# Kernel optimization log

Measured on AMD Instinct MI355X. Metric: run time of the kernel, lower is better.

Reference implementation:

```python
import jax, jax.numpy as jnp
import numpy as np


def setup_inputs() -> dict:
    key = jax.random.key(0)
    B, C, H, W = 16, 512, 56, 56
    heads, agent, win = 8, 49, 56
    ks = jax.random.split(key, 16)
    std = 0.02
    tn = lambda k, s: jax.random.truncated_normal(k, -2.0, 2.0, s, jnp.float32) * std
    return {
        "x": jax.random.normal(ks[0], (B, C, H, W), jnp.float32),
        "H": H,
        "W": W,
        "q_w": jax.random.normal(ks[1], (C, C), jnp.float32) * (C ** -0.5),
        "kv_w": jax.random.normal(ks[2], (2 * C, C), jnp.float32) * (C ** -0.5),
        "proj_w": jax.random.normal(ks[3], (C, C), jnp.float32) * (C ** -0.5),
        "proj_b": jnp.zeros((C,), jnp.float32),
        "dwc_w": jax.random.normal(ks[4], (C, 1, 3, 3), jnp.float32) * (1.0 / 3.0),
        "dwc_b": jnp.zeros((C,), jnp.float32),
        "an_bias": tn(ks[5], (heads, agent, 7, 7)),
        "na_bias": tn(ks[6], (heads, agent, 7, 7)),
        "ah_bias": tn(ks[7], (1, heads, agent, win, 1)),
        "aw_bias": tn(ks[8], (1, heads, agent, 1, win)),
        "ha_bias": tn(ks[9], (1, heads, win, 1, agent)),
        "wa_bias": tn(ks[10], (1, heads, 1, win, agent)),
    }


def reference(x, H, W, q_w, kv_w, proj_w, proj_b, dwc_w, dwc_b,
              an_bias, na_bias, ah_bias, aw_bias, ha_bias, wa_bias):
    B, C, H1, W1 = x.shape
    heads, agent = an_bias.shape[0], an_bias.shape[1]
    hd = C // heads
    scale = hd ** -0.5
    n = H1 * W1
    pool = int(agent ** 0.5)  # 7

    # NOTE: original torch code does x.view(B, H1*W1, C) on an NCHW tensor:
    # a raw row-major reshape, reproduced faithfully here.
    xf = x.reshape(B, n, C)

    q = xf @ q_w.T                       # [B, n, C]
    kv = xf @ kv_w.T                     # [B, n, 2C]
    k, v = kv[..., :C], kv[..., C:]

    # agent tokens: adaptive avg pool of q (as HxW image) to pool x pool (exact blocks)
    q_img = q.reshape(B, H, W, C)
    agent_tokens = q_img.reshape(B, pool, H // pool, pool, W // pool, C).mean(axis=(2, 4))
    agent_tokens = agent_tokens.reshape(B, agent, C)

    qh = q.reshape(B, n, heads, hd).transpose(0, 2, 1, 3)            # [B,h,n,d]
    kh = k.reshape(B, n, heads, hd).transpose(0, 2, 1, 3)            # [B,h,n,d]
    vh = v.reshape(B, n, heads, hd).transpose(0, 2, 1, 3)            # [B,h,n,d]
    ah = agent_tokens.reshape(B, agent, heads, hd).transpose(0, 2, 1, 3)  # [B,h,a,d]

    # stage 1: agent -> kv attention, with interpolated + separable position bias
    pb1 = jax.image.resize(an_bias, (heads, agent, H, W), 'bilinear').reshape(1, heads, agent, n)
    pb2 = (ah_bias + aw_bias).reshape(1, heads, agent, n)
    agent_logits = jnp.einsum('bhad,bhnd->bhan', ah * scale, kh) + pb1 + pb2
    agent_attn = jax.nn.softmax(agent_logits, axis=-1)
    agent_v = jnp.einsum('bhan,bhnd->bhad', agent_attn, vh)          # [B,h,a,d]

    # stage 2: query -> agent attention
    ab1 = jax.image.resize(na_bias, (heads, agent, H, W), 'bilinear').reshape(1, heads, agent, n)
    ab1 = ab1.transpose(0, 1, 3, 2)                                  # [1,h,n,a]
    ab2 = (ha_bias + wa_bias).reshape(1, heads, n, agent)
    q_logits = jnp.einsum('bhnd,bhad->bhna', qh * scale, ah) + ab1 + ab2
    q_attn = jax.nn.softmax(q_logits, axis=-1)
    out = jnp.einsum('bhna,bhad->bhnd', q_attn, agent_v)
    out = out.transpose(0, 2, 1, 3).reshape(B, n, C)

    # depthwise-conv residual on v (sr_ratio == 1: no interpolate)
    v_img = v.reshape(B, H, W, C).transpose(0, 3, 1, 2)              # [B,C,H,W]
    dwc = jax.lax.conv_general_dilated(
        v_img, dwc_w, window_strides=(1, 1), padding='SAME',
        feature_group_count=C, dimension_numbers=('NCHW', 'OIHW', 'NCHW'))
    dwc = dwc + dwc_b[None, :, None, None]
    out = out + dwc.transpose(0, 2, 3, 1).reshape(B, n, C)

    out = out @ proj_w.T + proj_b
    return out.reshape(B, C, H1, W1)
```

## Files before the change

### kernel.cpp

```cpp
#include <hip/hip_runtime.h>
#include <math.h>

#define B_ 16
#define C_ 512
#define Nn 3136
#define HEADS 8
#define HD 64
#define AG 49
#define Mrows (B_ * Nn)

typedef unsigned short ushortT;
typedef __attribute__((ext_vector_type(8))) short bf16x8;
typedef __attribute__((ext_vector_type(4))) float f32x4;

#define MFMA16(a, b, c) __builtin_amdgcn_mfma_f32_16x16x32_bf16((a), (b), (c), 0, 0, 0)

__device__ inline float bf2f(ushortT u) { return __uint_as_float(((unsigned)u) << 16); }
__device__ inline ushortT f2bf(float f) {
    unsigned x = __float_as_uint(f);
    unsigned r = (x + 0x7fffu + ((x >> 16) & 1u)) >> 16;
    return (ushortT)r;
}
__device__ inline f32x4 fzero4() { f32x4 z = {0.f, 0.f, 0.f, 0.f}; return z; }

__device__ inline void gl_lds16(const ushortT* g, ushortT* l) {
    __builtin_amdgcn_global_load_lds(
        (const __attribute__((address_space(1))) void*)g,
        (__attribute__((address_space(3))) void*)l, 16, 0, 0);
}

#define VMCNT(n) asm volatile("s_waitcnt vmcnt(" #n ")" ::: "memory")
#define LGKM0_SB() { asm volatile("s_waitcnt lgkmcnt(0)" ::: "memory"); \
                     __builtin_amdgcn_sched_barrier(0); }
#define BAR() __builtin_amdgcn_s_barrier()

__global__ void cvt_f2b4(const float* __restrict__ src, ushortT* __restrict__ dst, int n4) {
    int g = blockIdx.x * 256 + threadIdx.x;
    if (g >= n4) return;
    float4 v = *(const float4*)&src[(size_t)g * 4];
    ushort4 o = make_ushort4(f2bf(v.x), f2bf(v.y), f2bf(v.z), f2bf(v.w));
    *(ushort4*)&dst[(size_t)g * 4] = o;
}

__global__ void cvt_weights(const float* __restrict__ qw, const float* __restrict__ kvw,
                            const float* __restrict__ pw, const float* __restrict__ dwcw,
                            ushortT* __restrict__ Wqkv, ushortT* __restrict__ Wp,
                            float* __restrict__ wT) {
    int g = blockIdx.x * 256 + threadIdx.x;
    if (g < 196608) {
        const float* src = (g < 65536) ? &qw[(size_t)g * 4] : &kvw[(size_t)(g - 65536) * 4];
        float4 v = *(const float4*)src;
        *(ushort4*)&Wqkv[(size_t)g * 4] =
            make_ushort4(f2bf(v.x), f2bf(v.y), f2bf(v.z), f2bf(v.w));
    } else if (g < 262144) {
        float4 v = *(const float4*)&pw[(size_t)(g - 196608) * 4];
        *(ushort4*)&Wp[(size_t)(g - 196608) * 4] =
            make_ushort4(f2bf(v.x), f2bf(v.y), f2bf(v.z), f2bf(v.w));
    } else {
        int gg = g - 262144;
        if (gg < 4608) { int c = gg & 511, tap = gg >> 9; wT[gg] = dwcw[c * 9 + tap]; }
    }
}

template <int MB, int NL>
__device__ __forceinline__ void quad(f32x4 (&acc)[8][4], const bf16x8 (&af)[4][2],
                                     const bf16x8 (&bf)[4][2]) {
#pragma unroll
    for (int m = 0; m < 4; ++m)
#pragma unroll
        for (int n = 0; n < 2; ++n) {
            acc[MB + m][NL + n] = MFMA16(af[m][0], bf[NL + n][0], acc[MB + m][NL + n]);
            acc[MB + m][NL + n] = MFMA16(af[m][1], bf[NL + n][1], acc[MB + m][NL + n]);
        }
}

template <typename TO>
__global__ __launch_bounds__(512, 2)
void gemm256(const ushortT* __restrict__ A, const ushortT* __restrict__ Bw,
             const float* __restrict__ bias, TO* __restrict__ out,
             int N, int nbn) {
    __shared__ __align__(16) ushortT As[2][16384];
    __shared__ __align__(16) ushortT Bs[2][16384];
    const int t = threadIdx.x, lane = t & 63, wid = t >> 6;
    const int chunk = (int)gridDim.x >> 3;
    const int id2 = ((int)blockIdx.x & 7) * chunk + ((int)blockIdx.x >> 3);
    const int by = id2 / nbn, bx = id2 - by * nbn;
    const int m0 = by * 256, n0 = bx * 256;
    const int wm = wid >> 2, wn = wid & 3;

    const int rl0 = t >> 3;
    const int skg = (t & 7) ^ (rl0 & 7);
    const int ra0 = rl0 & 63;
    const int ra1 = (rl0 & 63) + 128;
    const int rb0 = (rl0 & 31) + ((rl0 >> 5) << 6);
    const int rb1 = rb0 + 128;
    const ushortT* gA0 = A + (size_t)(m0 + ra0) * 512 + skg * 8;
    const ushortT* gA1 = A + (size_t)(m0 + ra1) * 512 + skg * 8;
    const ushortT* gB0 = Bw + (size_t)(n0 + rb0) * 512 + skg * 8;
    const ushortT* gB1 = Bw + (size_t)(n0 + rb1) * 512 + skg * 8;
    const int bA0 = wid * 512;
    const int bA1 = wid * 512 + 8192;
    const int gbu = ((wid * 8) & 31) + (((wid * 8) >> 5) << 6);
    const int bB0 = gbu * 64;
    const int bB1 = bB0 + 8192;

#define ISSA(bufi, ro, ko) { gl_lds16(gA0 + (ro) * 512 + (ko), &As[bufi][bA0 + (ro) * 64]); \
                             gl_lds16(gA1 + (ro) * 512 + (ko), &As[bufi][bA1 + (ro) * 64]); }
#define ISSB(bufi, ro, ko) { gl_lds16(gB0 + (ro) * 512 + (ko), &Bs[bufi][bB0 + (ro) * 64]); \
                             gl_lds16(gB1 + (ro) * 512 + (ko), &Bs[bufi][bB1 + (ro) * 64]); }

    f32x4 acc[8][4];
#pragma unroll
    for (int i = 0; i < 8; ++i)
#pragma unroll
        for (int j = 0; j < 4; ++j) acc[i][j] = fzero4();

    const int r15 = lane & 15, kq16 = lane >> 4;
    const int rA = wm * 128 + r15;
    const int rB = wn * 64 + r15;
    const int sw0 = ((kq16) ^ (r15 & 7)) << 3;
    const int sw1 = ((4 + kq16) ^ (r15 & 7)) << 3;

    ISSA(0, 0, 0); ISSA(0, 64, 0);
    ISSB(0, 0, 0); ISSB(0, 32, 0);
    VMCNT(0);
    BAR();

    bf16x8 af[4][2], bf[4][2];
    for (int kt = 0; kt < 8; ++kt) {
        const ushortT* Ac = As[kt & 1];
        const ushortT* Bc = Bs[kt & 1];
        const int nb = (kt + 1) & 1;
        const int ko = (kt + 1) * 64;
        const bool pre = (kt < 7);
#pragma unroll
        for (int mt = 0; mt < 4; ++mt) {
            af[mt][0] = *(const bf16x8*)&Ac[(rA + mt * 16) * 64 + sw0];
            af[mt][1] = *(const bf16x8*)&Ac[(rA + mt * 16) * 64 + sw1];
        }
#pragma unroll
        for (int nt = 0; nt < 2; ++nt) {
            bf[nt][0] = *(const bf16x8*)&Bc[(rB + nt * 16) * 64 + sw0];
            bf[nt][1] = *(const bf16x8*)&Bc[(rB + nt * 16) * 64 + sw1];
        }
        if (pre) { ISSA(nb, 0, ko); ISSA(nb, 64, ko); }
        BAR(); LGKM0_SB();
        __builtin_amdgcn_s_setprio(1);
        quad<0, 0>(acc, af, bf);
        __builtin_amdgcn_s_setprio(0);
        BAR();
#pragma unroll
        for (int nt = 2; nt < 4; ++nt) {
            bf[nt][0] = *(const bf16x8*)&Bc[(rB + nt * 16) * 64 + sw0];
            bf[nt][1] = *(const bf16x8*)&Bc[(rB + nt * 16) * 64 + sw1];
        }
        if (pre) { ISSB(nb, 0, ko); ISSB(nb, 32, ko); }
        BAR(); LGKM0_SB();
        __builtin_amdgcn_s_setprio(1);
        quad<0, 2>(acc, af, bf);
        __builtin_amdgcn_s_setprio(0);
        BAR();
#pragma unroll
        for (int mt = 0; mt < 4; ++mt) {
            af[mt][0] = *(const bf16x8*)&Ac[(rA + 64 + mt * 16) * 64 + sw0];
            af[mt][1] = *(const bf16x8*)&Ac[(rA + 64 + mt * 16) * 64 + sw1];
        }
        BAR(); LGKM0_SB();
        __builtin_amdgcn_s_setprio(1);
        quad<4, 0>(acc, af, bf);
        __builtin_amdgcn_s_setprio(0);
        BAR();
        __builtin_amdgcn_s_setprio(1);
        quad<4, 2>(acc, af, bf);
        __builtin_amdgcn_s_setprio(0);
        if (pre) { VMCNT(0); }
        BAR();
    }
#undef ISSA
#undef ISSB

    const int cn = r15, rg = kq16 << 2;
#pragma unroll
    for (int mt = 0; mt < 8; ++mt) {
        int mrow = m0 + wm * 128 + mt * 16 + rg;
#pragma unroll
        for (int nt = 0; nt < 4; ++nt) {
            int ncol = n0 + wn * 64 + nt * 16 + cn;
            float bv = bias ? bias[ncol] : 0.f;
#pragma unroll
            for (int r = 0; r < 4; ++r) {
                float v = acc[mt][nt][r] + bv;
                if (sizeof(TO) == 2) ((ushortT*)out)[(size_t)(mrow + r) * N + ncol] = f2bf(v);
                else                 ((float*)out)[(size_t)(mrow + r) * N + ncol] = v;
            }
        }
    }
}

__global__ __launch_bounds__(256)
void agent_pool(const ushortT* __restrict__ qkv, float* __restrict__ at) {
    __shared__ float red[256][9];
    int t = threadIdx.x;
    int ba = blockIdx.x;
    int b = ba / AG, a = ba % AG;
    int c8 = (t & 63) << 3, qr = t >> 6;
    int p1 = a / 7, p2 = a % 7;
    float s[8] = {};
#pragma unroll
    for (int pp = 0; pp < 16; ++pp) {
        int pos = (qr << 4) + pp;
        int i = (p1 * 8 + (pos >> 3)) * 56 + p2 * 8 + (pos & 7);
        bf16x8 u = *(const bf16x8*)&qkv[(size_t)(b * Nn + i) * 1536 + c8];
#pragma unroll
        for (int j = 0; j < 8; ++j) s[j] += bf2f((ushortT)u[j]);
    }
#pragma unroll
    for (int j = 0; j < 8; ++j) red[t][j] = s[j];
    __syncthreads();
    if (t < 64) {
        float* o = &at[((size_t)(b * AG + a) << 9) + (t << 3)];
#pragma unroll
        for (int j = 0; j < 8; ++j)
            o[j] = (red[t][j] + red[t + 64][j] + red[t + 128][j] + red[t + 192][j])
                   * (1.f / 64.f);
    }
}

__device__ inline float bilin7(const float* __restrict__ p, int y, int x) {
    float fy = fminf(fmaxf(y * 0.125f - 0.4375f, 0.f), 6.f);
    float fx = fminf(fmaxf(x * 0.125f - 0.4375f, 0.f), 6.f);
    int y0 = (int)fy; float ty = fy - y0; int y1 = min(y0 + 1, 6);
    int x0 = (int)fx; float tx = fx - x0; int x1 = min(x0 + 1, 6);
    float v00 = p[y0 * 7 + x0], v01 = p[y0 * 7 + x1];
    float v10 = p[y1 * 7 + x0], v11 = p[y1 * 7 + x1];
    return (1.f - ty) * ((1.f - tx) * v00 + tx * v01) + ty * ((1.f - tx) * v10 + tx * v11);
}

__global__ void bias_k(const float* __restrict__ an, const float* __restrict__ ahb,
                       const float* __restrict__ awb, const float* __restrict__ na,
                       const float* __restrict__ hab, const float* __restrict__ wab,
                       float* __restrict__ b1, float* __restrict__ b2) {
    int g = blockIdx.x * 256 + threadIdx.x;
    const int NT = HEADS * AG * Nn;
    if (g < NT) {
        int i = g % Nn; int a = (g / Nn) % AG; int h = g / (AG * Nn);
        int y = i / 56, x = i % 56;
        b1[g] = bilin7(an + (h * AG + a) * 49, y, x)
              + ahb[(h * AG + a) * 56 + y] + awb[(h * AG + a) * 56 + x];
    } else {
        g -= NT; if (g >= NT) return;
        int a = g % AG; int i = (g / AG) % Nn; int h = g / (AG * Nn);
        int y = i / 56, x = i % 56;
        b2[g] = bilin7(na + (h * AG + a) * 49, y, x)
              + hab[(h * 56 + y) * AG + a] + wab[(h * 56 + x) * AG + a];
    }
}

__global__ void zero2(float* __restrict__ num, int n1, float* __restrict__ den, int n2) {
    int g = blockIdx.x * 256 + threadIdx.x;
    if (g < n1) num[g] = 0.f;
    else if (g - n1 < n2) den[g - n1] = 0.f;
}

__global__ __launch_bounds__(256)
void agent_av_fused(const ushortT* __restrict__ qkv, const float* __restrict__ at,
                    const float* __restrict__ b1, float* __restrict__ num,
                    float* __restrict__ den) {
    __shared__ __align__(16) ushortT ah_s[64 * 72];
    __shared__ __align__(16) ushortT vt[64 * 72];
    __shared__ __align__(16) ushortT p_s[64 * 72];
    const int t = threadIdx.x, lane = t & 63, wid = t >> 6;
    const int bh = blockIdx.y, b = bh >> 3, h = bh & 7;
    for (int idx = t; idx < 512; idx += 256) {
        int a = idx >> 3, d8 = (idx & 7) << 3;
        bf16x8 tmp;
        if (a < AG) {
            const float* p = &at[((size_t)(b * AG + a) << 9) + (h << 6) + d8];
#pragma unroll
            for (int j = 0; j < 8; ++j) tmp[j] = (short)f2bf(p[j] * 0.125f);
        } else {
#pragma unroll
            for (int j = 0; j < 8; ++j) tmp[j] = 0;
        }
        *(bf16x8*)&ah_s[a * 72 + d8] = tmp;
    }
    __syncthreads();
    const int r15 = lane & 15, kq = (lane >> 4) << 3;
    const int rbase = (lane >> 4) << 2;
    bf16x8 af[4][2];
#pragma unroll
    for (int mt = 0; mt < 4; ++mt)
#pragma unroll
        for (int ks = 0; ks < 2; ++ks)
            af[mt][ks] = *(const bf16x8*)&ah_s[(mt * 16 + r15) * 72 + ks * 32 + kq];

    f32x4 accn[4];
#pragma unroll
    for (int nt = 0; nt < 4; ++nt) accn[nt] = fzero4();
    float denl[4][4];
#pragma unroll
    for (int mt = 0; mt < 4; ++mt)
#pragma unroll
        for (int r = 0; r < 4; ++r) denl[mt][r] = 0.f;

    const int i0b = blockIdx.x * 448;
    const int svi = t >> 2, svd = (t & 3) << 4;
    for (int cc = 0; cc < 7; ++cc) {
        const int i0 = i0b + cc * 64;
        {
            const ushortT* vp = &qkv[(size_t)(b * Nn + i0 + svi) * 1536 + 1024 + (h << 6) + svd];
            bf16x8 u0 = *(const bf16x8*)vp;
            bf16x8 u1 = *(const bf16x8*)(vp + 8);
#pragma unroll
            for (int j = 0; j < 8; ++j) {
                vt[(svd + j) * 72 + svi]     = (ushortT)u0[j];
                vt[(svd + 8 + j) * 72 + svi] = (ushortT)u1[j];
            }
        }
        {
            const int iw = i0 + wid * 16;
            const ushortT* kp = &qkv[(size_t)(b * Nn + iw + r15) * 1536 + 512 + (h << 6) + kq];
            bf16x8 bk0 = *(const bf16x8*)kp;
            bf16x8 bk1 = *(const bf16x8*)(kp + 32);
            f32x4 sacc[4];
#pragma unroll
            for (int mt = 0; mt < 4; ++mt) {
                sacc[mt] = MFMA16(af[mt][0], bk0, fzero4());
                sacc[mt] = MFMA16(af[mt][1], bk1, sacc[mt]);
            }
            const int ic = iw + r15;
#pragma unroll
            for (int mt = 0; mt < 4; ++mt)
#pragma unroll
                for (int r = 0; r < 4; ++r) {
                    int a = mt * 16 + rbase + r;
                    float e = 0.f;
                    if (a < AG)
                        e = __expf(sacc[mt][r] + b1[(size_t)(h * AG + a) * Nn + ic]);
                    denl[mt][r] += e;
                    p_s[a * 72 + wid * 16 + r15] = f2bf(e);
                }
        }
        __syncthreads();
        {
            bf16x8 ap0 = *(const bf16x8*)&p_s[(wid * 16 + r15) * 72 + kq];
            bf16x8 ap1 = *(const bf16x8*)&p_s[(wid * 16 + r15) * 72 + 32 + kq];
#pragma unroll
            for (int nt = 0; nt < 4; ++nt) {
                bf16x8 bv0 = *(const bf16x8*)&vt[(nt * 16 + r15) * 72 + kq];
                bf16x8 bv1 = *(const bf16x8*)&vt[(nt * 16 + r15) * 72 + 32 + kq];
                accn[nt] = MFMA16(ap0, bv0, accn[nt]);
                accn[nt] = MFMA16(ap1, bv1, accn[nt]);
            }
        }
        __syncthreads();
    }
#pragma unroll
    for (int r = 0; r < 4; ++r) {
        int a = wid * 16 + rbase + r;
        if (a < AG) {
#pragma unroll
            for (int nt = 0; nt < 4; ++nt)
                atomicAdd(&num[((size_t)(bh * AG + a) << 6) + nt * 16 + r15],
                          accn[nt][r]);
        }
    }
#pragma unroll
    for (int mt = 0; mt < 4; ++mt)
#pragma unroll
        for (int r = 0; r < 4; ++r) {
            float s = denl[mt][r];
#pragma unroll
            for (int off = 8; off >= 1; off >>= 1) s += __shfl_xor(s, off);
            if (r15 == 0) {
                int a = mt * 16 + rbase + r;
                if (a < AG) atomicAdd(&den[bh * AG + a], s);
            }
        }
}

__global__ __launch_bounds__(256)
void q_attn_mfma(const ushortT* __restrict__ qkv, const float* __restrict__ at,
                 const float* __restrict__ num, const float* __restrict__ den,
                 const float* __restrict__ b2, ushortT* __restrict__ attn) {
    __shared__ __align__(16) ushortT ah_s[64 * 72];
    __shared__ __align__(16) ushortT avT[64 * 72];
    __shared__ __align__(16) ushortT p_s[4][16 * 72];
    int t = threadIdx.x, lane = t & 63, wid = t >> 6;
    int bh = blockIdx.y, b = bh >> 3, h = bh & 7;
    for (int idx = t; idx < 512; idx += 256) {
        int a = idx >> 3, d8 = (idx & 7) << 3;
        bf16x8 tmp;
        if (a < AG) {
            const float* p = &at[((size_t)(b * AG + a) << 9) + (h << 6) + d8];
#pragma unroll
            for (int j = 0; j < 8; ++j) tmp[j] = (short)f2bf(p[j] * 0.125f);
        } else {
#pragma unroll
            for (int j = 0; j < 8; ++j) tmp[j] = 0;
        }
        *(bf16x8*)&ah_s[a * 72 + d8] = tmp;
    }
    for (int idx = t; idx < 4096; idx += 256) {
        int a = idx >> 6, d = idx & 63;
        float v = 0.f;
        if (a < AG)
            v = num[((size_t)(bh * AG + a) << 6) + d] / den[bh * AG + a];
        avT[d * 72 + a] = f2bf(v);
    }
    __syncthreads();
    int r15 = lane & 15, kq = (lane >> 4) << 3;
    bf16x8 bah[4][2], bav[4][2];
#pragma unroll
    for (int nt = 0; nt < 4; ++nt)
#pragma unroll
        for (int ks = 0; ks < 2; ++ks) {
            bah[nt][ks] = *(const bf16x8*)&ah_s[(nt * 16 + r15) * 72 + ks * 32 + kq];
            bav[nt][ks] = *(const bf16x8*)&avT[(nt * 16 + r15) * 72 + ks * 32 + kq];
        }
    ushortT* psw = p_s[wid];
    int i0b = blockIdx.x * 448;
    int rbase = (lane >> 4) << 2;
    for (int tt = 0; tt < 7; ++tt) {
        int i0 = i0b + (wid * 7 + tt) * 16;
        const ushortT* qp = &qkv[(size_t)(b * Nn + i0 + r15) * 1536 + (h << 6) + kq];
        bf16x8 aq0 = *(const bf16x8*)qp;
        bf16x8 aq1 = *(const bf16x8*)(qp + 32);
        f32x4 lg[4];
#pragma unroll
        for (int nt = 0; nt < 4; ++nt) {
            lg[nt] = MFMA16(aq0, bah[nt][0], fzero4());
            lg[nt] = MFMA16(aq1, bah[nt][1], lg[nt]);
        }
        float p4[4][4];
#pragma unroll
        for (int r = 0; r < 4; ++r) {
            int i = i0 + rbase + r;
            float vals[4]; float sm = 0.f;
#pragma unroll
            for (int nt = 0; nt < 4; ++nt) {
                int a = nt * 16 + r15;
                float e = 0.f;
                if (a < AG) e = __expf(lg[nt][r] + b2[(size_t)(h * Nn + i) * AG + a]);
                vals[nt] = e; sm += e;
            }
#pragma unroll
            for (int off = 8; off >= 1; off >>= 1) sm += __shfl_xor(sm, off);
            float inv = 1.f / sm;
#pragma unroll
            for (int nt = 0; nt < 4; ++nt) p4[nt][r] = vals[nt] * inv;
        }
#pragma unroll
        for (int nt = 0; nt < 4; ++nt)
#pragma unroll
            for (int r = 0; r < 4; ++r)
                psw[(rbase + r) * 72 + nt * 16 + r15] = f2bf(p4[nt][r]);
        bf16x8 ap0 = *(const bf16x8*)&psw[r15 * 72 + kq];
        bf16x8 ap1 = *(const bf16x8*)&psw[r15 * 72 + 32 + kq];
        f32x4 ov[4];
#pragma unroll
        for (int nt = 0; nt < 4; ++nt) {
            ov[nt] = MFMA16(ap0, bav[nt][0], fzero4());
            ov[nt] = MFMA16(ap1, bav[nt][1], ov[nt]);
        }
#pragma unroll
        for (int r = 0; r < 4; ++r) {
            int i = i0 + rbase + r;
            ushortT* op = &attn[(size_t)(b * Nn + i) * C_ + (h << 6)];
#pragma unroll
            for (int nt = 0; nt < 4; ++nt)
                op[nt * 16 + r15] = f2bf(ov[nt][r]);
        }
    }
}

__global__ void dwc_add_v(const ushortT* __restrict__ qkv, const float* __restrict__ wT,
                          const float* __restrict__ bb, ushortT* __restrict__ attn) {
    int g = blockIdx.x * 256 + threadIdx.x;
    int c8 = (g & 63) << 3;
    int bi = g >> 6;
    int i = bi % Nn;
    int y = i / 56, x = i % 56;
    float acc[8];
    {
        float4 b0 = *(const float4*)&bb[c8];
        float4 b1 = *(const float4*)&bb[c8 + 4];
        acc[0] = b0.x; acc[1] = b0.y; acc[2] = b0.z; acc[3] = b0.w;
        acc[4] = b1.x; acc[5] = b1.y; acc[6] = b1.z; acc[7] = b1.w;
    }
#pragma unroll
    for (int dy = -1; dy <= 1; ++dy) {
        int yy = y + dy; if (yy < 0 || yy > 55) continue;
#pragma unroll
        for (int dx = -1; dx <= 1; ++dx) {
            int xx = x + dx; if (xx < 0 || xx > 55) continue;
            const ushortT* vp = &qkv[(size_t)(bi + dy * 56 + dx) * 1536 + 1024 + c8];
            ushort4 u0 = *(const ushort4*)vp;
            ushort4 u1 = *(const ushort4*)(vp + 4);
            const float* wp = &wT[((dy + 1) * 3 + dx + 1) * 512 + c8];
            float4 w0 = *(const float4*)wp;
            float4 w1 = *(const float4*)(wp + 4);
            acc[0] += bf2f(u0.x) * w0.x; acc[1] += bf2f(u0.y) * w0.y;
            acc[2] += bf2f(u0.z) * w0.z; acc[3] += bf2f(u0.w) * w0.w;
            acc[4] += bf2f(u1.x) * w1.x; acc[5] += bf2f(u1.y) * w1.y;
            acc[6] += bf2f(u1.z) * w1.z; acc[7] += bf2f(u1.w) * w1.w;
        }
    }
    ushortT* op = &attn[(size_t)bi * C_ + c8];
    ushort4 a0 = *(const ushort4*)op;
    ushort4 a1 = *(const ushort4*)(op + 4);
    ushort4 o0 = make_ushort4(f2bf(bf2f(a0.x) + acc[0]), f2bf(bf2f(a0.y) + acc[1]),
                              f2bf(bf2f(a0.z) + acc[2]), f2bf(bf2f(a0.w) + acc[3]));
    ushort4 o1 = make_ushort4(f2bf(bf2f(a1.x) + acc[4]), f2bf(bf2f(a1.y) + acc[5]),
                              f2bf(bf2f(a1.z) + acc[6]), f2bf(bf2f(a1.w) + acc[7]));
    *(ushort4*)op = o0; *(ushort4*)(op + 4) = o1;
}

extern "C" void kernel_launch(void* const* d_in, const int* in_sizes, int n_in,
                              void* d_out, int out_size, void* d_ws, size_t ws_size,
                              hipStream_t stream) {
    const float* x      = (const float*)d_in[0];
    const float* q_w    = (const float*)d_in[3];
    const float* kv_w   = (const float*)d_in[4];
    const float* proj_w = (const float*)d_in[5];
    const float* proj_b = (const float*)d_in[6];
    const float* dwc_w  = (const float*)d_in[7];
    const float* dwc_b  = (const float*)d_in[8];
    const float* an_b   = (const float*)d_in[9];
    const float* na_b   = (const float*)d_in[10];
    const float* ah_b   = (const float*)d_in[11];
    const float* aw_b   = (const float*)d_in[12];
    const float* ha_b   = (const float*)d_in[13];
    const float* wa_b   = (const float*)d_in[14];
    float* out = (float*)d_out;

    char* ws = (char*)d_ws;
    ushortT* R    = (ushortT*)(ws);
    ushortT* qkv  = (ushortT*)(ws + 51380224);
    ushortT* Wqkv = (ushortT*)(ws + 205520896);
    ushortT* Wp   = (ushortT*)(ws + 207093760);
    float*   wT   = (float*)(ws + 207618048);
    float*   at   = (float*)(ws + 207636480);
    float*   b1   = (float*)(ws + 209242112);
    float*   b2   = (float*)(ws + 214159360);
    float*   num  = (float*)(ws + 219076608);
    float*   den  = (float*)Wqkv;
    ushortT* xb   = R;
    ushortT* attn = R;

    cvt_f2b4<<<25088, 256, 0, stream>>>(x, xb, 6422528);
    cvt_weights<<<1042, 256, 0, stream>>>(q_w, kv_w, proj_w, dwc_w, Wqkv, Wp, wT);
    gemm256<ushortT><<<1176, 512, 0, stream>>>(xb, Wqkv, nullptr, qkv, 1536, 6);
    agent_pool<<<784, 256, 0, stream>>>(qkv, at);
    bias_k<<<9604, 256, 0, stream>>>(an_b, ah_b, aw_b, na_b, ha_b, wa_b, b1, b2);
    zero2<<<1593, 256, 0, stream>>>(num, B_ * HEADS * AG * HD, den, B_ * HEADS * AG);
    agent_av_fused<<<dim3(7, 128), 256, 0, stream>>>(qkv, at, b1, num, den);
    q_attn_mfma<<<dim3(7, 128), 256, 0, stream>>>(qkv, at, num, den, b2, attn);
    dwc_add_v<<<12544, 256, 0, stream>>>(qkv, wT, dwc_b, attn);
    gemm256<float><<<392, 512, 0, stream>>>(attn, Wp, proj_b, out, 512, 2);
}
```

Measured before the change: 527.5 us.

## Use 128x128 GEMM tiles, bf16 bias/agent buffers, and atomic-free partial reductions

Replaces the 256x256 eight-wave GEMM with a simpler 128x128 four-wave GEMM that has a single barrier per k-step and more blocks. Agent tokens and the bias tables are stored as bf16 instead of fp32, with the head scale folded into the pooling, which halves their memory traffic. The agent-attention kernel now writes per-chunk partial numerators and denominators instead of using atomics, so the zeroing kernel is removed and q_attn sums the four partials. The smaller GEMM tile lowers data reuse per block, and bf16 biases reduce accuracy slightly.

```diff
diff --git a/kernel.cpp b/kernel.cpp
--- a/kernel.cpp
+++ b/kernel.cpp
@@ -30,8 +30,6 @@
 }
 
 #define VMCNT(n) asm volatile("s_waitcnt vmcnt(" #n ")" ::: "memory")
-#define LGKM0_SB() { asm volatile("s_waitcnt lgkmcnt(0)" ::: "memory"); \
-                     __builtin_amdgcn_sched_barrier(0); }
 #define BAR() __builtin_amdgcn_s_barrier()
 
 __global__ void cvt_f2b4(const float* __restrict__ src, ushortT* __restrict__ dst, int n4) {
@@ -62,67 +60,49 @@
     }
 }
 
-template <int MB, int NL>
-__device__ __forceinline__ void quad(f32x4 (&acc)[8][4], const bf16x8 (&af)[4][2],
-                                     const bf16x8 (&bf)[4][2]) {
-#pragma unroll
-    for (int m = 0; m < 4; ++m)
-#pragma unroll
-        for (int n = 0; n < 2; ++n) {
-            acc[MB + m][NL + n] = MFMA16(af[m][0], bf[NL + n][0], acc[MB + m][NL + n]);
-            acc[MB + m][NL + n] = MFMA16(af[m][1], bf[NL + n][1], acc[MB + m][NL + n]);
-        }
-}
-
 template <typename TO>
-__global__ __launch_bounds__(512, 2)
-void gemm256(const ushortT* __restrict__ A, const ushortT* __restrict__ Bw,
+__global__ __launch_bounds__(256, 2)
+void gemm128(const ushortT* __restrict__ A, const ushortT* __restrict__ Bw,
              const float* __restrict__ bias, TO* __restrict__ out,
              int N, int nbn) {
-    __shared__ __align__(16) ushortT As[2][16384];
-    __shared__ __align__(16) ushortT Bs[2][16384];
+    __shared__ __align__(16) ushortT As[2][8192];
+    __shared__ __align__(16) ushortT Bs[2][8192];
     const int t = threadIdx.x, lane = t & 63, wid = t >> 6;
     const int chunk = (int)gridDim.x >> 3;
     const int id2 = ((int)blockIdx.x & 7) * chunk + ((int)blockIdx.x >> 3);
     const int by = id2 / nbn, bx = id2 - by * nbn;
-    const int m0 = by * 256, n0 = bx * 256;
-    const int wm = wid >> 2, wn = wid & 3;
-
-    const int rl0 = t >> 3;
-    const int skg = (t & 7) ^ (rl0 & 7);
-    const int ra0 = rl0 & 63;
-    const int ra1 = (rl0 & 63) + 128;
-    const int rb0 = (rl0 & 31) + ((rl0 >> 5) << 6);
-    const int rb1 = rb0 + 128;
-    const ushortT* gA0 = A + (size_t)(m0 + ra0) * 512 + skg * 8;
-    const ushortT* gA1 = A + (size_t)(m0 + ra1) * 512 + skg * 8;
-    const ushortT* gB0 = Bw + (size_t)(n0 + rb0) * 512 + skg * 8;
-    const ushortT* gB1 = Bw + (size_t)(n0 + rb1) * 512 + skg * 8;
-    const int bA0 = wid * 512;
-    const int bA1 = wid * 512 + 8192;
-    const int gbu = ((wid * 8) & 31) + (((wid * 8) >> 5) << 6);
-    const int bB0 = gbu * 64;
-    const int bB1 = bB0 + 8192;
-
-#define ISSA(bufi, ro, ko) { gl_lds16(gA0 + (ro) * 512 + (ko), &As[bufi][bA0 + (ro) * 64]); \
-                             gl_lds16(gA1 + (ro) * 512 + (ko), &As[bufi][bA1 + (ro) * 64]); }
-#define ISSB(bufi, ro, ko) { gl_lds16(gB0 + (ro) * 512 + (ko), &Bs[bufi][bB0 + (ro) * 64]); \
-                             gl_lds16(gB1 + (ro) * 512 + (ko), &Bs[bufi][bB1 + (ro) * 64]); }
-
-    f32x4 acc[8][4];
-#pragma unroll
-    for (int i = 0; i < 8; ++i)
+    const int m0 = by * 128, n0 = bx * 128;
+    const int wm = wid >> 1, wn = wid & 1;
+
+    const int srow = t >> 3;
+    const int skg = (t & 7) ^ (srow & 7);
+    const ushortT* gA = A + (size_t)(m0 + srow) * 512 + skg * 8;
+    const ushortT* gB = Bw + (size_t)(n0 + srow) * 512 + skg * 8;
+    const int dst = wid * 512;
+
+#define ISS(bufi, ko) { \
+    gl_lds16(gA + (ko),             &As[bufi][dst]); \
+    gl_lds16(gA + 16384 + (ko),     &As[bufi][2048 + dst]); \
+    gl_lds16(gA + 32768 + (ko),     &As[bufi][4096 + dst]); \
+    gl_lds16(gA + 49152 + (ko),     &As[bufi][6144 + dst]); \
+    gl_lds16(gB + (ko),             &Bs[bufi][dst]); \
+    gl_lds16(gB + 16384 + (ko),     &Bs[bufi][2048 + dst]); \
+    gl_lds16(gB + 32768 + (ko),     &Bs[bufi][4096 + dst]); \
+    gl_lds16(gB + 49152 + (ko),     &Bs[bufi][6144 + dst]); }
+
+    f32x4 acc[4][4];
+#pragma unroll
+    for (int i = 0; i < 4; ++i)
 #pragma unroll
         for (int j = 0; j < 4; ++j) acc[i][j] = fzero4();
 
     const int r15 = lane & 15, kq16 = lane >> 4;
-    const int rA = wm * 128 + r15;
+    const int rA = wm * 64 + r15;
     const int rB = wn * 64 + r15;
     const int sw0 = ((kq16) ^ (r15 & 7)) << 3;
     const int sw1 = ((4 + kq16) ^ (r15 & 7)) << 3;
 
-    ISSA(0, 0, 0); ISSA(0, 64, 0);
-    ISSB(0, 0, 0); ISSB(0, 32, 0);
+    ISS(0, 0);
     VMCNT(0);
     BAR();
 
@@ -130,59 +110,34 @@
     for (int kt = 0; kt < 8; ++kt) {
         const ushortT* Ac = As[kt & 1];
         const ushortT* Bc = Bs[kt & 1];
-        const int nb = (kt + 1) & 1;
-        const int ko = (kt + 1) * 64;
-        const bool pre = (kt < 7);
+        if (kt < 7) { const int nb = (kt + 1) & 1; const int ko = (kt + 1) * 64; ISS(nb, ko); }
 #pragma unroll
         for (int mt = 0; mt < 4; ++mt) {
             af[mt][0] = *(const bf16x8*)&Ac[(rA + mt * 16) * 64 + sw0];
             af[mt][1] = *(const bf16x8*)&Ac[(rA + mt * 16) * 64 + sw1];
         }
 #pragma unroll
-        for (int nt = 0; nt < 2; ++nt) {
+        for (int nt = 0; nt < 4; ++nt) {
             bf[nt][0] = *(const bf16x8*)&Bc[(rB + nt * 16) * 64 + sw0];
             bf[nt][1] = *(const bf16x8*)&Bc[(rB + nt * 16) * 64 + sw1];
         }
-        if (pre) { ISSA(nb, 0, ko); ISSA(nb, 64, ko); }
-        BAR(); LGKM0_SB();
         __builtin_amdgcn_s_setprio(1);
-        quad<0, 0>(acc, af, bf);
+#pragma unroll
+        for (int mt = 0; mt < 4; ++mt)
+#pragma unroll
+            for (int nt = 0; nt < 4; ++nt) {
+                acc[mt][nt] = MFMA16(af[mt][0], bf[nt][0], acc[mt][nt]);
+                acc[mt][nt] = MFMA16(af[mt][1], bf[nt][1], acc[mt][nt]);
+            }
         __builtin_amdgcn_s_setprio(0);
-        BAR();
-#pragma unroll
-        for (int nt = 2; nt < 4; ++nt) {
-            bf[nt][0] = *(const bf16x8*)&Bc[(rB + nt * 16) * 64 + sw0];
-            bf[nt][1] = *(const bf16x8*)&Bc[(rB + nt * 16) * 64 + sw1];
-        }
-        if (pre) { ISSB(nb, 0, ko); ISSB(nb, 32, ko); }
-        BAR(); LGKM0_SB();
-        __builtin_amdgcn_s_setprio(1);
-        quad<0, 2>(acc, af, bf);
-        __builtin_amdgcn_s_setprio(0);
-        BAR();
-#pragma unroll
-        for (int mt = 0; mt < 4; ++mt) {
-            af[mt][0] = *(const bf16x8*)&Ac[(rA + 64 + mt * 16) * 64 + sw0];
-            af[mt][1] = *(const bf16x8*)&Ac[(rA + 64 + mt * 16) * 64 + sw1];
-        }
-        BAR(); LGKM0_SB();
-        __builtin_amdgcn_s_setprio(1);
-        quad<4, 0>(acc, af, bf);
-        __builtin_amdgcn_s_setprio(0);
-        BAR();
-        __builtin_amdgcn_s_setprio(1);
-        quad<4, 2>(acc, af, bf);
-        __builtin_amdgcn_s_setprio(0);
-        if (pre) { VMCNT(0); }
-        BAR();
-    }
-#undef ISSA
-#undef ISSB
+        __syncthreads();
+    }
+#undef ISS
 
     const int cn = r15, rg = kq16 << 2;
 #pragma unroll
-    for (int mt = 0; mt < 8; ++mt) {
-        int mrow = m0 + wm * 128 + mt * 16 + rg;
+    for (int mt = 0; mt < 4; ++mt) {
+        int mrow = m0 + wm * 64 + mt * 16 + rg;
 #pragma unroll
         for (int nt = 0; nt < 4; ++nt) {
             int ncol = n0 + wn * 64 + nt * 16 + cn;
@@ -198,7 +153,7 @@
 }
 
 __global__ __launch_bounds__(256)
-void agent_pool(const ushortT* __restrict__ qkv, float* __restrict__ at) {
+void agent_pool(const ushortT* __restrict__ qkv, ushortT* __restrict__ at) {
     __shared__ float red[256][9];
     int t = threadIdx.x;
     int ba = blockIdx.x;
@@ -218,11 +173,11 @@
     for (int j = 0; j < 8; ++j) red[t][j] = s[j];
     __syncthreads();
     if (t < 64) {
-        float* o = &at[((size_t)(b * AG + a) << 9) + (t << 3)];
+        ushortT* o = &at[((size_t)(b * AG + a) << 9) + (t << 3)];
 #pragma unroll
         for (int j = 0; j < 8; ++j)
-            o[j] = (red[t][j] + red[t + 64][j] + red[t + 128][j] + red[t + 192][j])
-                   * (1.f / 64.f);
+            o[j] = f2bf((red[t][j] + red[t + 64][j] + red[t + 128][j] + red[t + 192][j])
+                        * (1.f / 512.f));
     }
 }
 
@@ -239,45 +194,39 @@
 __global__ void bias_k(const float* __restrict__ an, const float* __restrict__ ahb,
                        const float* __restrict__ awb, const float* __restrict__ na,
                        const float* __restrict__ hab, const float* __restrict__ wab,
-                       float* __restrict__ b1, float* __restrict__ b2) {
+                       ushortT* __restrict__ b1, ushortT* __restrict__ b2) {
     int g = blockIdx.x * 256 + threadIdx.x;
     const int NT = HEADS * AG * Nn;
     if (g < NT) {
         int i = g % Nn; int a = (g / Nn) % AG; int h = g / (AG * Nn);
         int y = i / 56, x = i % 56;
-        b1[g] = bilin7(an + (h * AG + a) * 49, y, x)
-              + ahb[(h * AG + a) * 56 + y] + awb[(h * AG + a) * 56 + x];
+        b1[g] = f2bf(bilin7(an + (h * AG + a) * 49, y, x)
+                     + ahb[(h * AG + a) * 56 + y] + awb[(h * AG + a) * 56 + x]);
     } else {
         g -= NT; if (g >= NT) return;
         int a = g % AG; int i = (g / AG) % Nn; int h = g / (AG * Nn);
         int y = i / 56, x = i % 56;
-        b2[g] = bilin7(na + (h * AG + a) * 49, y, x)
-              + hab[(h * 56 + y) * AG + a] + wab[(h * 56 + x) * AG + a];
-    }
-}
-
-__global__ void zero2(float* __restrict__ num, int n1, float* __restrict__ den, int n2) {
-    int g = blockIdx.x * 256 + threadIdx.x;
-    if (g < n1) num[g] = 0.f;
-    else if (g - n1 < n2) den[g - n1] = 0.f;
+        b2[g] = f2bf(bilin7(na + (h * AG + a) * 49, y, x)
+                     + hab[(h * 56 + y) * AG + a] + wab[(h * 56 + x) * AG + a]);
+    }
 }
 
 __global__ __launch_bounds__(256)
-void agent_av_fused(const ushortT* __restrict__ qkv, const float* __restrict__ at,
-                    const float* __restrict__ b1, float* __restrict__ num,
-                    float* __restrict__ den) {
+void agent_av_fused(const ushortT* __restrict__ qkv, const ushortT* __restrict__ at,
+                    const ushortT* __restrict__ b1, float* __restrict__ num_p,
+                    float* __restrict__ den_p) {
     __shared__ __align__(16) ushortT ah_s[64 * 72];
     __shared__ __align__(16) ushortT vt[64 * 72];
     __shared__ __align__(16) ushortT p_s[64 * 72];
     const int t = threadIdx.x, lane = t & 63, wid = t >> 6;
-    const int bh = blockIdx.y, b = bh >> 3, h = bh & 7;
+    const int bx = blockIdx.x, bh = blockIdx.y, b = bh >> 3, h = bh & 7;
+    const int cs = bx ? (13 + 12 * (bx - 1)) : 0;
+    const int ce = cs + (bx ? 12 : 13);
     for (int idx = t; idx < 512; idx += 256) {
         int a = idx >> 3, d8 = (idx & 7) << 3;
         bf16x8 tmp;
         if (a < AG) {
-            const float* p = &at[((size_t)(b * AG + a) << 9) + (h << 6) + d8];
-#pragma unroll
-            for (int j = 0; j < 8; ++j) tmp[j] = (short)f2bf(p[j] * 0.125f);
+            tmp = *(const bf16x8*)&at[((size_t)(b * AG + a) << 9) + (h << 6) + d8];
         } else {
 #pragma unroll
             for (int j = 0; j < 8; ++j) tmp[j] = 0;
@@ -303,10 +252,9 @@
 #pragma unroll
         for (int r = 0; r < 4; ++r) denl[mt][r] = 0.f;
 
-    const int i0b = blockIdx.x * 448;
     const int svi = t >> 2, svd = (t & 3) << 4;
-    for (int cc = 0; cc < 7; ++cc) {
-        const int i0 = i0b + cc * 64;
+    for (int cc = cs; cc < ce; ++cc) {
+        const int i0 = cc * 64;
         {
             const ushortT* vp = &qkv[(size_t)(b * Nn + i0 + svi) * 1536 + 1024 + (h << 6) + svd];
             bf16x8 u0 = *(const bf16x8*)vp;
@@ -336,7 +284,7 @@
                     int a = mt * 16 + rbase + r;
                     float e = 0.f;
                     if (a < AG)
-                        e = __expf(sacc[mt][r] + b1[(size_t)(h * AG + a) * Nn + ic]);
+                        e = __expf(sacc[mt][r] + bf2f(b1[(size_t)(h * AG + a) * Nn + ic]));
                     denl[mt][r] += e;
                     p_s[a * 72 + wid * 16 + r15] = f2bf(e);
                 }
@@ -361,10 +309,11 @@
         if (a < AG) {
 #pragma unroll
             for (int nt = 0; nt < 4; ++nt)
-                atomicAdd(&num[((size_t)(bh * AG + a) << 6) + nt * 16 + r15],
-                          accn[nt][r]);
-        }
-    }
+                num_p[(((size_t)bx * 128 + bh) * AG + a) * 64 + nt * 16 + r15] =
+                    accn[nt][r];
+        }
+    }
+    float* dsc = (float*)vt;
 #pragma unroll
     for (int mt = 0; mt < 4; ++mt)
 #pragma unroll
@@ -372,40 +321,52 @@
             float s = denl[mt][r];
 #pragma unroll
             for (int off = 8; off >= 1; off >>= 1) s += __shfl_xor(s, off);
-            if (r15 == 0) {
-                int a = mt * 16 + rbase + r;
-                if (a < AG) atomicAdd(&den[bh * AG + a], s);
-            }
-        }
+            if (r15 == 0) dsc[wid * 64 + mt * 16 + rbase + r] = s;
+        }
+    __syncthreads();
+    if (t < 64)
+        den_p[((size_t)bx * 128 + bh) * 64 + t] =
+            dsc[t] + dsc[64 + t] + dsc[128 + t] + dsc[192 + t];
 }
 
 __global__ __launch_bounds__(256)
-void q_attn_mfma(const ushortT* __restrict__ qkv, const float* __restrict__ at,
-                 const float* __restrict__ num, const float* __restrict__ den,
-                 const float* __restrict__ b2, ushortT* __restrict__ attn) {
+void q_attn_mfma(const ushortT* __restrict__ qkv, const ushortT* __restrict__ at,
+                 const float* __restrict__ num_p, const float* __restrict__ den_p,
+                 const ushortT* __restrict__ b2, ushortT* __restrict__ attn) {
     __shared__ __align__(16) ushortT ah_s[64 * 72];
     __shared__ __align__(16) ushortT avT[64 * 72];
     __shared__ __align__(16) ushortT p_s[4][16 * 72];
+    __shared__ float den_s[64];
     int t = threadIdx.x, lane = t & 63, wid = t >> 6;
     int bh = blockIdx.y, b = bh >> 3, h = bh & 7;
     for (int idx = t; idx < 512; idx += 256) {
         int a = idx >> 3, d8 = (idx & 7) << 3;
         bf16x8 tmp;
         if (a < AG) {
-            const float* p = &at[((size_t)(b * AG + a) << 9) + (h << 6) + d8];
-#pragma unroll
-            for (int j = 0; j < 8; ++j) tmp[j] = (short)f2bf(p[j] * 0.125f);
+            tmp = *(const bf16x8*)&at[((size_t)(b * AG + a) << 9) + (h << 6) + d8];
         } else {
 #pragma unroll
             for (int j = 0; j < 8; ++j) tmp[j] = 0;
         }
         *(bf16x8*)&ah_s[a * 72 + d8] = tmp;
     }
+    if (t < 64) {
+        den_s[t] = den_p[((size_t)0 * 128 + bh) * 64 + t]
+                 + den_p[((size_t)1 * 128 + bh) * 64 + t]
+                 + den_p[((size_t)2 * 128 + bh) * 64 + t]
+                 + den_p[((size_t)3 * 128 + bh) * 64 + t];
+    }
+    __syncthreads();
     for (int idx = t; idx < 4096; idx += 256) {
         int a = idx >> 6, d = idx & 63;
         float v = 0.f;
-        if (a < AG)
-            v = num[((size_t)(bh * AG + a) << 6) + d] / den[bh * AG + a];
+        if (a < AG) {
+            float s = num_p[(((size_t)0 * 128 + bh) * AG + a) * 64 + d]
+                    + num_p[(((size_t)1 * 128 + bh) * AG + a) * 64 + d]
+                    + num_p[(((size_t)2 * 128 + bh) * AG + a) * 64 + d]
+                    + num_p[(((size_t)3 * 128 + bh) * AG + a) * 64 + d];
+            v = s / den_s[a];
+        }
         avT[d * 72 + a] = f2bf(v);
     }
     __syncthreads();
@@ -441,7 +402,8 @@
             for (int nt = 0; nt < 4; ++nt) {
                 int a = nt * 16 + r15;
                 float e = 0.f;
-                if (a < AG) e = __expf(lg[nt][r] + b2[(size_t)(h * Nn + i) * AG + a]);
+                if (a < AG)
+                    e = __expf(lg[nt][r] + bf2f(b2[(size_t)(h * Nn + i) * AG + a]));
                 vals[nt] = e; sm += e;
             }
 #pragma unroll
@@ -535,27 +497,26 @@
     float* out = (float*)d_out;
 
     char* ws = (char*)d_ws;
-    ushortT* R    = (ushortT*)(ws);
-    ushortT* qkv  = (ushortT*)(ws + 51380224);
-    ushortT* Wqkv = (ushortT*)(ws + 205520896);
-    ushortT* Wp   = (ushortT*)(ws + 207093760);
-    float*   wT   = (float*)(ws + 207618048);
-    float*   at   = (float*)(ws + 207636480);
-    float*   b1   = (float*)(ws + 209242112);
-    float*   b2   = (float*)(ws + 214159360);
-    float*   num  = (float*)(ws + 219076608);
-    float*   den  = (float*)Wqkv;
-    ushortT* xb   = R;
-    ushortT* attn = R;
+    ushortT* R     = (ushortT*)(ws);
+    ushortT* qkv   = (ushortT*)(ws + 51380224);
+    ushortT* Wqkv  = (ushortT*)(ws + 205520896);
+    ushortT* Wp    = (ushortT*)(ws + 207093760);
+    float*   wT    = (float*)(ws + 207618048);
+    ushortT* at    = (ushortT*)(ws + 207636480);
+    ushortT* b1    = (ushortT*)(ws + 208439296);
+    ushortT* b2    = (ushortT*)(ws + 210897920);
+    float*   num_p = (float*)(ws + 213356544);
+    float*   den_p = (float*)(ws + 219779072);
+    ushortT* xb    = R;
+    ushortT* attn  = R;
 
     cvt_f2b4<<<25088, 256, 0, stream>>>(x, xb, 6422528);
     cvt_weights<<<1042, 256, 0, stream>>>(q_w, kv_w, proj_w, dwc_w, Wqkv, Wp, wT);
-    gemm256<ushortT><<<1176, 512, 0, stream>>>(xb, Wqkv, nullptr, qkv, 1536, 6);
+    gemm128<ushortT><<<4704, 256, 0, stream>>>(xb, Wqkv, nullptr, qkv, 1536, 12);
     agent_pool<<<784, 256, 0, stream>>>(qkv, at);
     bias_k<<<9604, 256, 0, stream>>>(an_b, ah_b, aw_b, na_b, ha_b, wa_b, b1, b2);
-    zero2<<<1593, 256, 0, stream>>>(num, B_ * HEADS * AG * HD, den, B_ * HEADS * AG);
-    agent_av_fused<<<dim3(7, 128), 256, 0, stream>>>(qkv, at, b1, num, den);
-    q_attn_mfma<<<dim3(7, 128), 256, 0, stream>>>(qkv, at, num, den, b2, attn);
+    agent_av_fused<<<dim3(4, 128), 256, 0, stream>>>(qkv, at, b1, num_p, den_p);
+    q_attn_mfma<<<dim3(7, 128), 256, 0, stream>>>(qkv, at, num_p, den_p, b2, attn);
     dwc_add_v<<<12544, 256, 0, stream>>>(qkv, wT, dwc_b, attn);
-    gemm256<float><<<392, 512, 0, stream>>>(attn, Wp, proj_b, out, 512, 2);
-}
+    gemm128<float><<<1568, 256, 0, stream>>>(attn, Wp, proj_b, out, 512, 4);
+}
```

Result: faster. 496.9 us (-5.8%).
